# Kernel optimization log

Hardware: AMD Instinct MI355X
Metric: run time of the kernel (lower is better)

Reference implementation:

```python
import jax, jax.numpy as jnp
import numpy as np

NUM_EMBEDDINGS = 512
EMBEDDING_DIM = 64
COMMITMENT_COST = 0.25


def setup_inputs() -> dict:
    key = jax.random.key(0)
    k1, k2 = jax.random.split(key)
    inputs = jax.random.normal(k1, (32, EMBEDDING_DIM, 64, 64), dtype=jnp.float32)  # NCHW
    # nn.Embedding weight init: uniform(-1/K, 1/K)
    embedding = jax.random.uniform(
        k2, (NUM_EMBEDDINGS, EMBEDDING_DIM), dtype=jnp.float32,
        minval=-1.0 / NUM_EMBEDDINGS, maxval=1.0 / NUM_EMBEDDINGS)
    return {"inputs": inputs, "embedding": embedding}


def reference(inputs, embedding):
    # NCHW -> NHWC, flatten to [N, D]
    x = jnp.transpose(inputs, (0, 2, 3, 1))
    flat = x.reshape(-1, EMBEDDING_DIM)  # [N, D]
    distances = (jnp.sum(flat * flat, axis=1, keepdims=True)
                 + jnp.sum(embedding * embedding, axis=1)
                 - 2.0 * flat @ embedding.T)
    idx = jnp.argmin(distances, axis=1)  # [N]
    # gather codebook rows (equivalent to one-hot @ embedding, fused)
    quantized = jnp.take(embedding, idx, axis=0).reshape(x.shape)
    e_latent_loss = jnp.mean((jax.lax.stop_gradient(quantized) - x) ** 2)
    q_latent_loss = jnp.mean((quantized - jax.lax.stop_gradient(x)) ** 2)
    loss = q_latent_loss + COMMITMENT_COST * e_latent_loss
    # straight-through estimator
    quantized = x + jax.lax.stop_gradient(quantized - x)
    out = jnp.transpose(quantized, (0, 3, 1, 2))  # back to NCHW
    return out, loss
```

## Files before the change

### kernel.cpp

```cpp
#include <hip/hip_runtime.h>


#define D 64
#define K_EMB 512
#define HW 4096
#define CHW (D * HW)
#define OUT_ELEMS 8388608
#define NB_MAIN 1024
#define SWZ(r) ((((r) ^ ((r) >> 2))) & 7)

typedef __attribute__((ext_vector_type(8))) short short8;
typedef __attribute__((ext_vector_type(4))) float f32x4;

__device__ __forceinline__ unsigned short f2bf(float f) {
    unsigned u = __float_as_uint(f);
    u += 0x7FFFu + ((u >> 16) & 1u);
    return (unsigned short)(u >> 16);
}
__device__ __forceinline__ float bf2f(unsigned short h) {
    return __uint_as_float(((unsigned)h) << 16);
}
__device__ __forceinline__ unsigned umin32(unsigned a, unsigned b) { return a <= b ? a : b; }
__device__ __forceinline__ unsigned cvtpk(float lo, float hi) {
    unsigned r;
    asm("v_cvt_pk_bf16_f32 %0, %1, %2" : "=v"(r) : "v"(lo), "v"(hi));
    return r;
}

__global__ void vq_prep(const float* __restrict__ emb, unsigned short* __restrict__ ebf,
                        float* __restrict__ npm) {
    int k = blockIdx.x * 256 + threadIdx.x;
    const float4* e4 = reinterpret_cast<const float4*>(emb + k * D);
    unsigned short h[D];
    float acc = 0.f;
#pragma unroll
    for (int i = 0; i < 16; ++i) {
        float4 v = e4[i];
        acc += v.x * v.x + v.y * v.y + v.z * v.z + v.w * v.w;
        h[4 * i + 0] = f2bf(v.x); h[4 * i + 1] = f2bf(v.y);
        h[4 * i + 2] = f2bf(v.z); h[4 * i + 3] = f2bf(v.w);
    }
    npm[k] = -0.5f * (1.0f + acc);
    uint4* dst = reinterpret_cast<uint4*>(ebf + k * D);
#pragma unroll
    for (int i = 0; i < 8; ++i) {
        uint4 p;
        p.x = (unsigned)h[8 * i + 0] | ((unsigned)h[8 * i + 1] << 16);
        p.y = (unsigned)h[8 * i + 2] | ((unsigned)h[8 * i + 3] << 16);
        p.z = (unsigned)h[8 * i + 4] | ((unsigned)h[8 * i + 5] << 16);
        p.w = (unsigned)h[8 * i + 6] | ((unsigned)h[8 * i + 7] << 16);
        dst[i] = p;
    }
}

__global__ __launch_bounds__(256, 4) void vq_mfma(const float* __restrict__ in,
                                                  const unsigned short* __restrict__ ebf,
                                                  const float* __restrict__ npm,
                                                  const float* __restrict__ emb,
                                                  float* __restrict__ out,
                                                  float* __restrict__ partials) {
    __shared__ __align__(16) char ldsX[16384];
    __shared__ __align__(16) unsigned keysS[4][128];
    __shared__ float red4[4];

    const int tid = threadIdx.x;
    const int lane = tid & 63;
    const int w = tid >> 6;
    const int col = lane & 15;
    const int dg = lane >> 4;
    const int bid = ((blockIdx.x & 7) << 7) | (blockIdx.x >> 3);
    const int n = bid >> 5;
    const int hw0 = (bid & 31) << 7;

    {
        const int rw = (tid & 31) * 4;
        const int cg = tid >> 5;
        const float* xb = in + n * CHW + cg * 8 * HW + hw0 + rw;
        f32x4 v[8];
#pragma unroll
        for (int ch = 0; ch < 8; ++ch)
            v[ch] = *reinterpret_cast<const f32x4*>(xb + ch * HW);
#pragma unroll
        for (int j = 0; j < 4; ++j) {
            const int r = rw + j;
            uint4 p;
            p.x = cvtpk(v[0][j], v[1][j]);
            p.y = cvtpk(v[2][j], v[3][j]);
            p.z = cvtpk(v[4][j], v[5][j]);
            p.w = cvtpk(v[6][j], v[7][j]);
            *reinterpret_cast<uint4*>(ldsX + r * 128 + ((cg ^ SWZ(r)) * 16)) = p;
        }
    }

    unsigned best[8][4];
#pragma unroll
    for (int rt = 0; rt < 8; ++rt)
#pragma unroll
        for (int i = 0; i < 4; ++i) best[rt][i] = 0xFFFFFFFFu;

    const short8* e8 = reinterpret_cast<const short8*>(ebf);
#pragma unroll 1
    for (int g = 0; g < 2; ++g) {
        const int kb = w * 128 + g * 64 + col;
        short8 ef[4][2];
        float npv[4];
#pragma unroll
        for (int ct = 0; ct < 4; ++ct) {
            const int k = kb + ct * 16;
            ef[ct][0] = e8[k * 8 + dg];
            ef[ct][1] = e8[k * 8 + 4 + dg];
            npv[ct] = npm[k];
        }
        if (g == 0) __syncthreads();

#pragma unroll
        for (int rt = 0; rt < 8; ++rt) {
            const int row = rt * 16 + col;
            short8 a0 = *reinterpret_cast<const short8*>(
                ldsX + row * 128 + ((dg ^ SWZ(row)) * 16));
            short8 a1 = *reinterpret_cast<const short8*>(
                ldsX + row * 128 + (((4 + dg) ^ SWZ(row)) * 16));
#pragma unroll
            for (int ct = 0; ct < 4; ++ct) {
                f32x4 acc = {npv[ct], npv[ct], npv[ct], npv[ct]};
                acc = __builtin_amdgcn_mfma_f32_16x16x32_bf16(a0, ef[ct][0], acc, 0, 0, 0);
                acc = __builtin_amdgcn_mfma_f32_16x16x32_bf16(a1, ef[ct][1], acc, 0, 0, 0);
                const unsigned kc = (unsigned)(kb + ct * 16);
#pragma unroll
                for (int i = 0; i < 4; ++i) {
                    unsigned key = (__float_as_uint(acc[i]) & 0xFFFFFE00u) | kc;
                    best[rt][i] = umin32(best[rt][i], key);
                }
            }
        }
    }

#pragma unroll
    for (int rt = 0; rt < 8; ++rt)
#pragma unroll
        for (int i = 0; i < 4; ++i) {
            unsigned k = best[rt][i];
#pragma unroll
            for (int s = 1; s < 16; s <<= 1)
                k = umin32(k, (unsigned)__shfl_xor((int)k, s, 64));
            if (col == 0) keysS[w][rt * 16 + dg * 4 + i] = k;
        }
    __syncthreads();

    const int rg = tid & 31;
    const int cs = tid >> 5;
    uint4 q0 = *reinterpret_cast<const uint4*>(&keysS[0][rg * 4]);
    uint4 q1 = *reinterpret_cast<const uint4*>(&keysS[1][rg * 4]);
    uint4 q2 = *reinterpret_cast<const uint4*>(&keysS[2][rg * 4]);
    uint4 q3 = *reinterpret_cast<const uint4*>(&keysS[3][rg * 4]);
    int kk[4];
    kk[0] = (int)(umin32(umin32(q0.x, q1.x), umin32(q2.x, q3.x)) & 511u);
    kk[1] = (int)(umin32(umin32(q0.y, q1.y), umin32(q2.y, q3.y)) & 511u);
    kk[2] = (int)(umin32(umin32(q0.z, q1.z), umin32(q2.z, q3.z)) & 511u);
    kk[3] = (int)(umin32(umin32(q0.w, q1.w), umin32(q2.w, q3.w)) & 511u);
    float ej[4][8];
#pragma unroll
    for (int j = 0; j < 4; ++j) {
        const f32x4* ep = reinterpret_cast<const f32x4*>(emb + kk[j] * D + cs * 8);
        *reinterpret_cast<f32x4*>(&ej[j][0]) = ep[0];
        *reinterpret_cast<f32x4*>(&ej[j][4]) = ep[1];
    }
    float lsum = 0.f;
#pragma unroll
    for (int j = 0; j < 4; ++j) {
        const int r = rg * 4 + j;
        short8 x8 = *reinterpret_cast<const short8*>(
            ldsX + r * 128 + ((cs ^ SWZ(r)) * 16));
#pragma unroll
        for (int t = 0; t < 8; ++t) {
            float d = ej[j][t] - bf2f((unsigned short)x8[t]);
            lsum = fmaf(d, d, lsum);
        }
    }
    float* obase = out + n * CHW + hw0 + rg * 4;
#pragma unroll
    for (int t = 0; t < 8; ++t) {
        f32x4 st = {ej[0][t], ej[1][t], ej[2][t], ej[3][t]};
        __builtin_nontemporal_store(st, reinterpret_cast<f32x4*>(obase + (cs * 8 + t) * HW));
    }

#pragma unroll
    for (int s = 1; s < 64; s <<= 1) lsum += __shfl_xor(lsum, s, 64);
    if (lane == 0) red4[w] = lsum;
    __syncthreads();
    if (tid == 0) partials[bid] = red4[0] + red4[1] + red4[2] + red4[3];
}

__global__ void vq_finalize(const float* __restrict__ partials, float* __restrict__ loss) {
    __shared__ float s[256];
    float a = 0.f;
    for (int i = threadIdx.x; i < NB_MAIN; i += 256) a += partials[i];
    s[threadIdx.x] = a;
    __syncthreads();
    for (int t = 128; t > 0; t >>= 1) {
        if ((int)threadIdx.x < t) s[threadIdx.x] += s[threadIdx.x + t];
        __syncthreads();
    }
    if (threadIdx.x == 0) loss[0] = 1.25f * s[0] * (1.0f / (float)OUT_ELEMS);
}

extern "C" void kernel_launch(void* const* d_in, const int* in_sizes, int n_in,
                              void* d_out, int out_size, void* d_ws, size_t ws_size,
                              hipStream_t stream) {
    const float* in = (const float*)d_in[0];
    const float* emb = (const float*)d_in[1];
    float* out = (float*)d_out;
    unsigned short* ebf = (unsigned short*)d_ws;
    float* npm = (float*)((char*)d_ws + 65536);
    float* partials = (float*)((char*)d_ws + 67584);

    vq_prep<<<2, 256, 0, stream>>>(emb, ebf, npm);
    vq_mfma<<<NB_MAIN, 256, 0, stream>>>(in, ebf, npm, emb, out, partials);
    vq_finalize<<<1, 256, 0, stream>>>(partials, out + OUT_ELEMS);
}
```

Baseline: 33.06 us.

## Double block tile to 256 rows with 8 waves each owning 64 codes

Each block now handles 256 spatial positions with 512 threads (8 waves), and each wave holds a fixed 64-code slice of the bf16 codebook in registers instead of looping over two 64-code groups. The running-min state shrinks to one row tile at a time, which lowers register pressure, and the cross-wave key reduction widens to 8 waves. The aim is to halve the number of blocks and codebook reloads per block and to raise parallelism per block. The cost is doubled LDS use (32 KB plus keys), which may limit occupancy, and only 512 blocks for the whole GPU.

Result: slower. 37.95 us (+14.8%).

```diff
diff --git a/kernel.cpp b/kernel.cpp
--- a/kernel.cpp
+++ b/kernel.cpp
@@ -6,7 +6,7 @@
 #define HW 4096
 #define CHW (D * HW)
 #define OUT_ELEMS 8388608
-#define NB_MAIN 1024
+#define NB_MAIN 512
 #define SWZ(r) ((((r) ^ ((r) >> 2))) & 7)
 
 typedef __attribute__((ext_vector_type(8))) short short8;
@@ -53,36 +53,36 @@
     }
 }
 
-__global__ __launch_bounds__(256, 4) void vq_mfma(const float* __restrict__ in,
+__global__ __launch_bounds__(512, 4) void vq_mfma(const float* __restrict__ in,
                                                   const unsigned short* __restrict__ ebf,
                                                   const float* __restrict__ npm,
                                                   const float* __restrict__ emb,
                                                   float* __restrict__ out,
                                                   float* __restrict__ partials) {
-    __shared__ __align__(16) char ldsX[16384];
-    __shared__ __align__(16) unsigned keysS[4][128];
-    __shared__ float red4[4];
+    __shared__ __align__(16) char ldsX[32768];
+    __shared__ __align__(16) unsigned keysS[8][256];
+    __shared__ float red8[8];
 
     const int tid = threadIdx.x;
     const int lane = tid & 63;
     const int w = tid >> 6;
     const int col = lane & 15;
     const int dg = lane >> 4;
-    const int bid = ((blockIdx.x & 7) << 7) | (blockIdx.x >> 3);
-    const int n = bid >> 5;
-    const int hw0 = (bid & 31) << 7;
+    const int bid = ((blockIdx.x & 7) << 6) | (blockIdx.x >> 3);
+    const int n = bid >> 4;
+    const int hw0 = (bid & 15) << 8;
 
     {
-        const int rw = (tid & 31) * 4;
-        const int cg = tid >> 5;
-        const float* xb = in + n * CHW + cg * 8 * HW + hw0 + rw;
+        const int pg = tid & 63;
+        const int cg = tid >> 6;
+        const float* xb = in + n * CHW + cg * 8 * HW + hw0 + pg * 4;
         f32x4 v[8];
 #pragma unroll
         for (int ch = 0; ch < 8; ++ch)
             v[ch] = *reinterpret_cast<const f32x4*>(xb + ch * HW);
 #pragma unroll
         for (int j = 0; j < 4; ++j) {
-            const int r = rw + j;
+            const int r = pg * 4 + j;
             uint4 p;
             p.x = cvtpk(v[0][j], v[1][j]);
             p.y = cvtpk(v[2][j], v[3][j]);
@@ -92,18 +92,11 @@
         }
     }
 
-    unsigned best[8][4];
-#pragma unroll
-    for (int rt = 0; rt < 8; ++rt)
-#pragma unroll
-        for (int i = 0; i < 4; ++i) best[rt][i] = 0xFFFFFFFFu;
-
-    const short8* e8 = reinterpret_cast<const short8*>(ebf);
-#pragma unroll 1
-    for (int g = 0; g < 2; ++g) {
-        const int kb = w * 128 + g * 64 + col;
-        short8 ef[4][2];
-        float npv[4];
+    const int kb = w * 64 + col;
+    short8 ef[4][2];
+    float npv[4];
+    {
+        const short8* e8 = reinterpret_cast<const short8*>(ebf);
 #pragma unroll
         for (int ct = 0; ct < 4; ++ct) {
             const int k = kb + ct * 16;
@@ -111,53 +104,56 @@
             ef[ct][1] = e8[k * 8 + 4 + dg];
             npv[ct] = npm[k];
         }
-        if (g == 0) __syncthreads();
-
-#pragma unroll
-        for (int rt = 0; rt < 8; ++rt) {
-            const int row = rt * 16 + col;
-            short8 a0 = *reinterpret_cast<const short8*>(
-                ldsX + row * 128 + ((dg ^ SWZ(row)) * 16));
-            short8 a1 = *reinterpret_cast<const short8*>(
-                ldsX + row * 128 + (((4 + dg) ^ SWZ(row)) * 16));
-#pragma unroll
-            for (int ct = 0; ct < 4; ++ct) {
-                f32x4 acc = {npv[ct], npv[ct], npv[ct], npv[ct]};
-                acc = __builtin_amdgcn_mfma_f32_16x16x32_bf16(a0, ef[ct][0], acc, 0, 0, 0);
-                acc = __builtin_amdgcn_mfma_f32_16x16x32_bf16(a1, ef[ct][1], acc, 0, 0, 0);
-                const unsigned kc = (unsigned)(kb + ct * 16);
-#pragma unroll
-                for (int i = 0; i < 4; ++i) {
-                    unsigned key = (__float_as_uint(acc[i]) & 0xFFFFFE00u) | kc;
-                    best[rt][i] = umin32(best[rt][i], key);
-                }
+    }
+    __syncthreads();
+
+#pragma unroll
+    for (int rt = 0; rt < 16; ++rt) {
+        const int row = rt * 16 + col;
+        short8 a0 = *reinterpret_cast<const short8*>(
+            ldsX + row * 128 + ((dg ^ SWZ(row)) * 16));
+        short8 a1 = *reinterpret_cast<const short8*>(
+            ldsX + row * 128 + (((4 + dg) ^ SWZ(row)) * 16));
+        unsigned best[4];
+#pragma unroll
+        for (int i = 0; i < 4; ++i) best[i] = 0xFFFFFFFFu;
+#pragma unroll
+        for (int ct = 0; ct < 4; ++ct) {
+            f32x4 acc = {npv[ct], npv[ct], npv[ct], npv[ct]};
+            acc = __builtin_amdgcn_mfma_f32_16x16x32_bf16(a0, ef[ct][0], acc, 0, 0, 0);
+            acc = __builtin_amdgcn_mfma_f32_16x16x32_bf16(a1, ef[ct][1], acc, 0, 0, 0);
+            const unsigned kc = (unsigned)(kb + ct * 16);
+#pragma unroll
+            for (int i = 0; i < 4; ++i) {
+                unsigned key = (__float_as_uint(acc[i]) & 0xFFFFFE00u) | kc;
+                best[i] = umin32(best[i], key);
             }
         }
-    }
-
-#pragma unroll
-    for (int rt = 0; rt < 8; ++rt)
 #pragma unroll
         for (int i = 0; i < 4; ++i) {
-            unsigned k = best[rt][i];
+            unsigned k = best[i];
 #pragma unroll
             for (int s = 1; s < 16; s <<= 1)
                 k = umin32(k, (unsigned)__shfl_xor((int)k, s, 64));
             if (col == 0) keysS[w][rt * 16 + dg * 4 + i] = k;
         }
-    __syncthreads();
-
-    const int rg = tid & 31;
-    const int cs = tid >> 5;
-    uint4 q0 = *reinterpret_cast<const uint4*>(&keysS[0][rg * 4]);
-    uint4 q1 = *reinterpret_cast<const uint4*>(&keysS[1][rg * 4]);
-    uint4 q2 = *reinterpret_cast<const uint4*>(&keysS[2][rg * 4]);
-    uint4 q3 = *reinterpret_cast<const uint4*>(&keysS[3][rg * 4]);
-    int kk[4];
-    kk[0] = (int)(umin32(umin32(q0.x, q1.x), umin32(q2.x, q3.x)) & 511u);
-    kk[1] = (int)(umin32(umin32(q0.y, q1.y), umin32(q2.y, q3.y)) & 511u);
-    kk[2] = (int)(umin32(umin32(q0.z, q1.z), umin32(q2.z, q3.z)) & 511u);
-    kk[3] = (int)(umin32(umin32(q0.w, q1.w), umin32(q2.w, q3.w)) & 511u);
+    }
+    __syncthreads();
+
+    const int rg = tid & 63;
+    const int cs = tid >> 6;
+    unsigned m0, m1, m2, m3;
+    {
+        uint4 q = *reinterpret_cast<const uint4*>(&keysS[0][rg * 4]);
+        m0 = q.x; m1 = q.y; m2 = q.z; m3 = q.w;
+    }
+#pragma unroll
+    for (int qw = 1; qw < 8; ++qw) {
+        uint4 q = *reinterpret_cast<const uint4*>(&keysS[qw][rg * 4]);
+        m0 = umin32(m0, q.x); m1 = umin32(m1, q.y);
+        m2 = umin32(m2, q.z); m3 = umin32(m3, q.w);
+    }
+    int kk[4] = {(int)(m0 & 511u), (int)(m1 & 511u), (int)(m2 & 511u), (int)(m3 & 511u)};
     float ej[4][8];
 #pragma unroll
     for (int j = 0; j < 4; ++j) {
@@ -186,9 +182,14 @@
 
 #pragma unroll
     for (int s = 1; s < 64; s <<= 1) lsum += __shfl_xor(lsum, s, 64);
-    if (lane == 0) red4[w] = lsum;
-    __syncthreads();
-    if (tid == 0) partials[bid] = red4[0] + red4[1] + red4[2] + red4[3];
+    if (lane == 0) red8[w] = lsum;
+    __syncthreads();
+    if (tid == 0) {
+        float p = 0.f;
+#pragma unroll
+        for (int q = 0; q < 8; ++q) p += red8[q];
+        partials[bid] = p;
+    }
 }
 
 __global__ void vq_finalize(const float* __restrict__ partials, float* __restrict__ loss) {
@@ -215,6 +216,6 @@
     float* partials = (float*)((char*)d_ws + 67584);
 
     vq_prep<<<2, 256, 0, stream>>>(emb, ebf, npm);
-    vq_mfma<<<NB_MAIN, 256, 0, stream>>>(in, ebf, npm, emb, out, partials);
+    vq_mfma<<<NB_MAIN, 512, 0, stream>>>(in, ebf, npm, emb, out, partials);
     vq_finalize<<<1, 256, 0, stream>>>(partials, out + OUT_ELEMS);
 }
```

## Process two tiles per block with prefetch of next tile's input

Applied to the files above, without the earlier changes.

Halves the grid so each block handles two 128-pixel tiles. The second tile's global loads are issued before the first tile's compute, and each tile gets its own LDS buffer. The per-row argmin reduction is moved inside the row loop and goes through shared-memory slots, which reduces live registers. Launch bounds drop to 2 blocks per CU, so occupancy and latency hiding may fall.

Measured after the change: 50.96 us. 1.54x slower.

```diff
diff --git a/kernel.cpp b/kernel.cpp
--- a/kernel.cpp
+++ b/kernel.cpp
@@ -6,7 +6,7 @@
 #define HW 4096
 #define CHW (D * HW)
 #define OUT_ELEMS 8388608
-#define NB_MAIN 1024
+#define NB_MAIN 512
 #define SWZ(r) ((((r) ^ ((r) >> 2))) & 7)
 
 typedef __attribute__((ext_vector_type(8))) short short8;
@@ -53,13 +53,13 @@
     }
 }
 
-__global__ __launch_bounds__(256, 4) void vq_mfma(const float* __restrict__ in,
+__global__ __launch_bounds__(256, 2) void vq_mfma(const float* __restrict__ in,
                                                   const unsigned short* __restrict__ ebf,
                                                   const float* __restrict__ npm,
                                                   const float* __restrict__ emb,
                                                   float* __restrict__ out,
                                                   float* __restrict__ partials) {
-    __shared__ __align__(16) char ldsX[16384];
+    __shared__ __align__(16) char ldsX[2][16384];
     __shared__ __align__(16) unsigned keysS[4][128];
     __shared__ float red4[4];
 
@@ -68,18 +68,31 @@
     const int w = tid >> 6;
     const int col = lane & 15;
     const int dg = lane >> 4;
-    const int bid = ((blockIdx.x & 7) << 7) | (blockIdx.x >> 3);
-    const int n = bid >> 5;
-    const int hw0 = (bid & 31) << 7;
-
+    const int bid = ((blockIdx.x & 7) << 6) | (blockIdx.x >> 3);
+
+    const int rw = (tid & 31) * 4;
+    const int cg = tid >> 5;
+
+    float lsum_all = 0.f;
+
+    f32x4 v[8];
     {
-        const int rw = (tid & 31) * 4;
-        const int cg = tid >> 5;
-        const float* xb = in + n * CHW + cg * 8 * HW + hw0 + rw;
-        f32x4 v[8];
+        const int tt = bid * 2;
+        const float* xb = in + (tt >> 5) * CHW + cg * 8 * HW + ((tt & 31) << 7) + rw;
 #pragma unroll
         for (int ch = 0; ch < 8; ++ch)
             v[ch] = *reinterpret_cast<const f32x4*>(xb + ch * HW);
+    }
+
+    const short8* e8 = reinterpret_cast<const short8*>(ebf);
+
+#pragma unroll 1
+    for (int tn = 0; tn < 2; ++tn) {
+        const int tt = bid * 2 + tn;
+        const int n = tt >> 5;
+        const int hw0 = (tt & 31) << 7;
+        char* X = ldsX[tn];
+
 #pragma unroll
         for (int j = 0; j < 4; ++j) {
             const int r = rw + j;
@@ -88,105 +101,104 @@
             p.y = cvtpk(v[2][j], v[3][j]);
             p.z = cvtpk(v[4][j], v[5][j]);
             p.w = cvtpk(v[6][j], v[7][j]);
-            *reinterpret_cast<uint4*>(ldsX + r * 128 + ((cg ^ SWZ(r)) * 16)) = p;
-        }
-    }
-
-    unsigned best[8][4];
-#pragma unroll
-    for (int rt = 0; rt < 8; ++rt)
-#pragma unroll
-        for (int i = 0; i < 4; ++i) best[rt][i] = 0xFFFFFFFFu;
-
-    const short8* e8 = reinterpret_cast<const short8*>(ebf);
+            *reinterpret_cast<uint4*>(X + r * 128 + ((cg ^ SWZ(r)) * 16)) = p;
+        }
+        if (tn == 0) {
+            const int t2 = tt + 1;
+            const float* xb2 = in + (t2 >> 5) * CHW + cg * 8 * HW + ((t2 & 31) << 7) + rw;
+#pragma unroll
+            for (int ch = 0; ch < 8; ++ch)
+                v[ch] = *reinterpret_cast<const f32x4*>(xb2 + ch * HW);
+        }
+        __syncthreads();
+
 #pragma unroll 1
-    for (int g = 0; g < 2; ++g) {
-        const int kb = w * 128 + g * 64 + col;
-        short8 ef[4][2];
-        float npv[4];
-#pragma unroll
-        for (int ct = 0; ct < 4; ++ct) {
-            const int k = kb + ct * 16;
-            ef[ct][0] = e8[k * 8 + dg];
-            ef[ct][1] = e8[k * 8 + 4 + dg];
-            npv[ct] = npm[k];
-        }
-        if (g == 0) __syncthreads();
-
-#pragma unroll
-        for (int rt = 0; rt < 8; ++rt) {
-            const int row = rt * 16 + col;
-            short8 a0 = *reinterpret_cast<const short8*>(
-                ldsX + row * 128 + ((dg ^ SWZ(row)) * 16));
-            short8 a1 = *reinterpret_cast<const short8*>(
-                ldsX + row * 128 + (((4 + dg) ^ SWZ(row)) * 16));
+        for (int g = 0; g < 2; ++g) {
+            const int kb = w * 128 + g * 64 + col;
+            short8 ef[4][2];
+            float npv[4];
 #pragma unroll
             for (int ct = 0; ct < 4; ++ct) {
-                f32x4 acc = {npv[ct], npv[ct], npv[ct], npv[ct]};
-                acc = __builtin_amdgcn_mfma_f32_16x16x32_bf16(a0, ef[ct][0], acc, 0, 0, 0);
-                acc = __builtin_amdgcn_mfma_f32_16x16x32_bf16(a1, ef[ct][1], acc, 0, 0, 0);
-                const unsigned kc = (unsigned)(kb + ct * 16);
+                const int k = kb + ct * 16;
+                ef[ct][0] = e8[k * 8 + dg];
+                ef[ct][1] = e8[k * 8 + 4 + dg];
+                npv[ct] = npm[k];
+            }
+#pragma unroll
+            for (int rt = 0; rt < 8; ++rt) {
+                const int row = rt * 16 + col;
+                short8 a0 = *reinterpret_cast<const short8*>(
+                    X + row * 128 + ((dg ^ SWZ(row)) * 16));
+                short8 a1 = *reinterpret_cast<const short8*>(
+                    X + row * 128 + (((4 + dg) ^ SWZ(row)) * 16));
+                unsigned best[4] = {0xFFFFFFFFu, 0xFFFFFFFFu, 0xFFFFFFFFu, 0xFFFFFFFFu};
+#pragma unroll
+                for (int ct = 0; ct < 4; ++ct) {
+                    f32x4 acc = {npv[ct], npv[ct], npv[ct], npv[ct]};
+                    acc = __builtin_amdgcn_mfma_f32_16x16x32_bf16(a0, ef[ct][0], acc, 0, 0, 0);
+                    acc = __builtin_amdgcn_mfma_f32_16x16x32_bf16(a1, ef[ct][1], acc, 0, 0, 0);
+                    const unsigned kc = (unsigned)(kb + ct * 16);
+#pragma unroll
+                    for (int i = 0; i < 4; ++i) {
+                        unsigned key = (__float_as_uint(acc[i]) & 0xFFFFFE00u) | kc;
+                        best[i] = umin32(best[i], key);
+                    }
+                }
 #pragma unroll
                 for (int i = 0; i < 4; ++i) {
-                    unsigned key = (__float_as_uint(acc[i]) & 0xFFFFFE00u) | kc;
-                    best[rt][i] = umin32(best[rt][i], key);
+                    unsigned k = best[i];
+#pragma unroll
+                    for (int s = 1; s < 16; s <<= 1)
+                        k = umin32(k, (unsigned)__shfl_xor((int)k, s, 64));
+                    if (col == 0) {
+                        unsigned* slot = &keysS[w][rt * 16 + dg * 4 + i];
+                        *slot = g == 0 ? k : umin32(*slot, k);
+                    }
                 }
             }
         }
-    }
-
-#pragma unroll
-    for (int rt = 0; rt < 8; ++rt)
-#pragma unroll
-        for (int i = 0; i < 4; ++i) {
-            unsigned k = best[rt][i];
-#pragma unroll
-            for (int s = 1; s < 16; s <<= 1)
-                k = umin32(k, (unsigned)__shfl_xor((int)k, s, 64));
-            if (col == 0) keysS[w][rt * 16 + dg * 4 + i] = k;
-        }
-    __syncthreads();
-
-    const int rg = tid & 31;
-    const int cs = tid >> 5;
-    uint4 q0 = *reinterpret_cast<const uint4*>(&keysS[0][rg * 4]);
-    uint4 q1 = *reinterpret_cast<const uint4*>(&keysS[1][rg * 4]);
-    uint4 q2 = *reinterpret_cast<const uint4*>(&keysS[2][rg * 4]);
-    uint4 q3 = *reinterpret_cast<const uint4*>(&keysS[3][rg * 4]);
-    int kk[4];
-    kk[0] = (int)(umin32(umin32(q0.x, q1.x), umin32(q2.x, q3.x)) & 511u);
-    kk[1] = (int)(umin32(umin32(q0.y, q1.y), umin32(q2.y, q3.y)) & 511u);
-    kk[2] = (int)(umin32(umin32(q0.z, q1.z), umin32(q2.z, q3.z)) & 511u);
-    kk[3] = (int)(umin32(umin32(q0.w, q1.w), umin32(q2.w, q3.w)) & 511u);
-    float ej[4][8];
-#pragma unroll
-    for (int j = 0; j < 4; ++j) {
-        const f32x4* ep = reinterpret_cast<const f32x4*>(emb + kk[j] * D + cs * 8);
-        *reinterpret_cast<f32x4*>(&ej[j][0]) = ep[0];
-        *reinterpret_cast<f32x4*>(&ej[j][4]) = ep[1];
-    }
-    float lsum = 0.f;
-#pragma unroll
-    for (int j = 0; j < 4; ++j) {
-        const int r = rg * 4 + j;
-        short8 x8 = *reinterpret_cast<const short8*>(
-            ldsX + r * 128 + ((cs ^ SWZ(r)) * 16));
+        __syncthreads();
+
+        const int rg = tid & 31;
+        const int cs = tid >> 5;
+        uint4 q0 = *reinterpret_cast<const uint4*>(&keysS[0][rg * 4]);
+        uint4 q1 = *reinterpret_cast<const uint4*>(&keysS[1][rg * 4]);
+        uint4 q2 = *reinterpret_cast<const uint4*>(&keysS[2][rg * 4]);
+        uint4 q3 = *reinterpret_cast<const uint4*>(&keysS[3][rg * 4]);
+        int kk[4];
+        kk[0] = (int)(umin32(umin32(q0.x, q1.x), umin32(q2.x, q3.x)) & 511u);
+        kk[1] = (int)(umin32(umin32(q0.y, q1.y), umin32(q2.y, q3.y)) & 511u);
+        kk[2] = (int)(umin32(umin32(q0.z, q1.z), umin32(q2.z, q3.z)) & 511u);
+        kk[3] = (int)(umin32(umin32(q0.w, q1.w), umin32(q2.w, q3.w)) & 511u);
+        float ej[4][8];
+#pragma unroll
+        for (int j = 0; j < 4; ++j) {
+            const f32x4* ep = reinterpret_cast<const f32x4*>(emb + kk[j] * D + cs * 8);
+            *reinterpret_cast<f32x4*>(&ej[j][0]) = ep[0];
+            *reinterpret_cast<f32x4*>(&ej[j][4]) = ep[1];
+        }
+#pragma unroll
+        for (int j = 0; j < 4; ++j) {
+            const int r = rg * 4 + j;
+            short8 x8 = *reinterpret_cast<const short8*>(
+                X + r * 128 + ((cs ^ SWZ(r)) * 16));
+#pragma unroll
+            for (int t = 0; t < 8; ++t) {
+                float d = ej[j][t] - bf2f((unsigned short)x8[t]);
+                lsum_all = fmaf(d, d, lsum_all);
+            }
+        }
+        float* obase = out + n * CHW + hw0 + rg * 4;
 #pragma unroll
         for (int t = 0; t < 8; ++t) {
-            float d = ej[j][t] - bf2f((unsigned short)x8[t]);
-            lsum = fmaf(d, d, lsum);
-        }
-    }
-    float* obase = out + n * CHW + hw0 + rg * 4;
-#pragma unroll
-    for (int t = 0; t < 8; ++t) {
-        f32x4 st = {ej[0][t], ej[1][t], ej[2][t], ej[3][t]};
-        __builtin_nontemporal_store(st, reinterpret_cast<f32x4*>(obase + (cs * 8 + t) * HW));
-    }
-
-#pragma unroll
-    for (int s = 1; s < 64; s <<= 1) lsum += __shfl_xor(lsum, s, 64);
-    if (lane == 0) red4[w] = lsum;
+            f32x4 st = {ej[0][t], ej[1][t], ej[2][t], ej[3][t]};
+            __builtin_nontemporal_store(st, reinterpret_cast<f32x4*>(obase + (cs * 8 + t) * HW));
+        }
+    }
+
+#pragma unroll
+    for (int s = 1; s < 64; s <<= 1) lsum_all += __shfl_xor(lsum_all, s, 64);
+    if (lane == 0) red4[w] = lsum_all;
     __syncthreads();
     if (tid == 0) partials[bid] = red4[0] + red4[1] + red4[2] + red4[3];
 }
```

## Split argmin and output scatter into separate kernels via index buffer

Applied to the files above, without the earlier changes.

The main kernel now only computes argmin indices and loss partials and writes 16-bit indices to workspace. A new scatter kernel stages an 8-channel slice of the codebook in LDS, gathers rows by index and writes the NCHW output with wide nontemporal stores. The loss finalization is folded into block 0 of the scatter kernel, so the separate finalize launch is gone. The aim is to take the output writes off the MFMA kernel's critical path. The cost is an extra index round-trip through memory and some re-reading of the codebook per block.

Result: slower. 48.71 us (+47.3%).

```diff
diff --git a/kernel.cpp b/kernel.cpp
--- a/kernel.cpp
+++ b/kernel.cpp
@@ -11,6 +11,7 @@
 
 typedef __attribute__((ext_vector_type(8))) short short8;
 typedef __attribute__((ext_vector_type(4))) float f32x4;
+typedef __attribute__((ext_vector_type(4))) unsigned short us4;
 
 __device__ __forceinline__ unsigned short f2bf(float f) {
     unsigned u = __float_as_uint(f);
@@ -53,12 +54,12 @@
     }
 }
 
-__global__ __launch_bounds__(256, 4) void vq_mfma(const float* __restrict__ in,
-                                                  const unsigned short* __restrict__ ebf,
-                                                  const float* __restrict__ npm,
-                                                  const float* __restrict__ emb,
-                                                  float* __restrict__ out,
-                                                  float* __restrict__ partials) {
+__global__ __launch_bounds__(256, 4) void vq_argmin(const float* __restrict__ in,
+                                                    const unsigned short* __restrict__ ebf,
+                                                    const float* __restrict__ npm,
+                                                    const float* __restrict__ emb,
+                                                    unsigned short* __restrict__ idxb,
+                                                    float* __restrict__ partials) {
     __shared__ __align__(16) char ldsX[16384];
     __shared__ __align__(16) unsigned keysS[4][128];
     __shared__ float red4[4];
@@ -158,6 +159,11 @@
     kk[1] = (int)(umin32(umin32(q0.y, q1.y), umin32(q2.y, q3.y)) & 511u);
     kk[2] = (int)(umin32(umin32(q0.z, q1.z), umin32(q2.z, q3.z)) & 511u);
     kk[3] = (int)(umin32(umin32(q0.w, q1.w), umin32(q2.w, q3.w)) & 511u);
+    if (cs == 0) {
+        us4 iv = {(unsigned short)kk[0], (unsigned short)kk[1],
+                  (unsigned short)kk[2], (unsigned short)kk[3]};
+        *reinterpret_cast<us4*>(idxb + bid * 128 + rg * 4) = iv;
+    }
     float ej[4][8];
 #pragma unroll
     for (int j = 0; j < 4; ++j) {
@@ -177,13 +183,6 @@
             lsum = fmaf(d, d, lsum);
         }
     }
-    float* obase = out + n * CHW + hw0 + rg * 4;
-#pragma unroll
-    for (int t = 0; t < 8; ++t) {
-        f32x4 st = {ej[0][t], ej[1][t], ej[2][t], ej[3][t]};
-        __builtin_nontemporal_store(st, reinterpret_cast<f32x4*>(obase + (cs * 8 + t) * HW));
-    }
-
 #pragma unroll
     for (int s = 1; s < 64; s <<= 1) lsum += __shfl_xor(lsum, s, 64);
     if (lane == 0) red4[w] = lsum;
@@ -191,17 +190,66 @@
     if (tid == 0) partials[bid] = red4[0] + red4[1] + red4[2] + red4[3];
 }
 
-__global__ void vq_finalize(const float* __restrict__ partials, float* __restrict__ loss) {
-    __shared__ float s[256];
-    float a = 0.f;
-    for (int i = threadIdx.x; i < NB_MAIN; i += 256) a += partials[i];
-    s[threadIdx.x] = a;
+__global__ __launch_bounds__(256, 4) void vq_scatter(const float* __restrict__ emb,
+                                                     const unsigned short* __restrict__ idxb,
+                                                     const float* __restrict__ partials,
+                                                     float* __restrict__ out) {
+    __shared__ __align__(16) float eC[K_EMB][8];
+    __shared__ float fin[256];
+
+    const int tid = threadIdx.x;
+    const int bid = blockIdx.x;
+    const int n = bid >> 4;
+    const int cg = (bid >> 1) & 7;
+    const int half = bid & 1;
+
+#pragma unroll
+    for (int q = 0; q < 2; ++q) {
+        const int k = tid + q * 256;
+        f32x4 a = *reinterpret_cast<const f32x4*>(emb + k * D + cg * 8);
+        f32x4 b = *reinterpret_cast<const f32x4*>(emb + k * D + cg * 8 + 4);
+        *reinterpret_cast<f32x4*>(&eC[k][0]) = a;
+        *reinterpret_cast<f32x4*>(&eC[k][4]) = b;
+    }
     __syncthreads();
-    for (int t = 128; t > 0; t >>= 1) {
-        if ((int)threadIdx.x < t) s[threadIdx.x] += s[threadIdx.x + t];
+
+    const int px0 = half * 2048 + tid * 8;
+    us4 i01 = *reinterpret_cast<const us4*>(idxb + n * HW + px0);
+    us4 i23 = *reinterpret_cast<const us4*>(idxb + n * HW + px0 + 4);
+    float vv[8][8];
+#pragma unroll
+    for (int p = 0; p < 4; ++p) {
+        const int k = (int)i01[p];
+        *reinterpret_cast<f32x4*>(&vv[p][0]) = *reinterpret_cast<const f32x4*>(&eC[k][0]);
+        *reinterpret_cast<f32x4*>(&vv[p][4]) = *reinterpret_cast<const f32x4*>(&eC[k][4]);
+    }
+#pragma unroll
+    for (int p = 0; p < 4; ++p) {
+        const int k = (int)i23[p];
+        *reinterpret_cast<f32x4*>(&vv[4 + p][0]) = *reinterpret_cast<const f32x4*>(&eC[k][0]);
+        *reinterpret_cast<f32x4*>(&vv[4 + p][4]) = *reinterpret_cast<const f32x4*>(&eC[k][4]);
+    }
+    float* ob = out + n * CHW + cg * 8 * HW + px0;
+#pragma unroll
+    for (int c = 0; c < 8; ++c) {
+        f32x4 s0 = {vv[0][c], vv[1][c], vv[2][c], vv[3][c]};
+        f32x4 s1 = {vv[4][c], vv[5][c], vv[6][c], vv[7][c]};
+        __builtin_nontemporal_store(s0, reinterpret_cast<f32x4*>(ob + c * HW));
+        __builtin_nontemporal_store(s1, reinterpret_cast<f32x4*>(ob + c * HW + 4));
+    }
+
+    if (bid == 0) {
+        float a = 0.f;
+#pragma unroll
+        for (int i = 0; i < 4; ++i) a += partials[tid + 256 * i];
+        fin[tid] = a;
         __syncthreads();
-    }
-    if (threadIdx.x == 0) loss[0] = 1.25f * s[0] * (1.0f / (float)OUT_ELEMS);
+        for (int t = 128; t > 0; t >>= 1) {
+            if (tid < t) fin[tid] += fin[tid + t];
+            __syncthreads();
+        }
+        if (tid == 0) out[OUT_ELEMS] = 1.25f * fin[0] * (1.0f / (float)OUT_ELEMS);
+    }
 }
 
 extern "C" void kernel_launch(void* const* d_in, const int* in_sizes, int n_in,
@@ -213,8 +261,9 @@
     unsigned short* ebf = (unsigned short*)d_ws;
     float* npm = (float*)((char*)d_ws + 65536);
     float* partials = (float*)((char*)d_ws + 67584);
+    unsigned short* idxb = (unsigned short*)((char*)d_ws + 73728);
 
     vq_prep<<<2, 256, 0, stream>>>(emb, ebf, npm);
-    vq_mfma<<<NB_MAIN, 256, 0, stream>>>(in, ebf, npm, emb, out, partials);
-    vq_finalize<<<1, 256, 0, stream>>>(partials, out + OUT_ELEMS);
-}
+    vq_argmin<<<NB_MAIN, 256, 0, stream>>>(in, ebf, npm, emb, idxb, partials);
+    vq_scatter<<<512, 256, 0, stream>>>(emb, idxb, partials, out);
+}
```
